# Kernel tuning notes

Measured on AMD Instinct MI355X. Metric: run time of the kernel, lower is better.

The kernel has to match this reference:

```python
import jax, jax.numpy as jnp
import numpy as np


def _dequant_linear(x, wq, scale):
    # wq: int [out, in], scale: [out] per-output-channel
    w = wq.astype(jnp.float32) * scale[:, None]  # dequantize
    return jnp.einsum('bsh,oh->bso', x, w)


def setup_inputs() -> dict:
    key = jax.random.key(0)
    ks = jax.random.split(key, 7)
    B, S, H, I = 2, 2048, 4096, 14336
    x = jax.random.normal(ks[0], (B, S, H), dtype=jnp.float32)
    gate_wq = jax.random.randint(ks[1], (I, H), -128, 128, dtype=jnp.int32)
    up_wq = jax.random.randint(ks[2], (I, H), -128, 128, dtype=jnp.int32)
    down_wq = jax.random.randint(ks[3], (H, I), -128, 128, dtype=jnp.int32)
    # small positive per-channel scales (~1/(127*sqrt(fan_in)))
    gate_scale = jax.random.uniform(ks[4], (I,), dtype=jnp.float32, minval=0.5, maxval=1.5) / (127.0 * np.sqrt(H))
    up_scale = jax.random.uniform(ks[5], (I,), dtype=jnp.float32, minval=0.5, maxval=1.5) / (127.0 * np.sqrt(H))
    down_scale = jax.random.uniform(ks[6], (H,), dtype=jnp.float32, minval=0.5, maxval=1.5) / (127.0 * np.sqrt(I))
    return {'x': x, 'gate_wq': gate_wq, 'gate_scale': gate_scale,
            'up_wq': up_wq, 'up_scale': up_scale,
            'down_wq': down_wq, 'down_scale': down_scale}


def reference(x, gate_wq, gate_scale, up_wq, up_scale, down_wq, down_scale):
    gate = _dequant_linear(x, gate_wq, gate_scale)   # [B,S,I]
    up = _dequant_linear(x, up_wq, up_scale)         # [B,S,I]
    h = jax.nn.silu(gate) * up                       # SwiGLU
    return _dequant_linear(h, down_wq, down_scale)   # [B,S,H]
```

## Files before the change

kernel.cpp:

```cpp
#include <hip/hip_runtime.h>

typedef __bf16 bf16x8 __attribute__((ext_vector_type(8)));
typedef float f32x4 __attribute__((ext_vector_type(4)));

__device__ __forceinline__ unsigned short f2bf(float f) {
  unsigned u = __float_as_uint(f);
  u += 0x7FFFu + ((u >> 16) & 1u);
  return (unsigned short)(u >> 16);
}

__device__ __forceinline__ void async16(const void* g, void* l) {
  __builtin_amdgcn_global_load_lds((const __attribute__((address_space(1))) void*)g,
                                   (__attribute__((address_space(3))) void*)l,
                                   16, 0, 0);
}

__global__ void cvt_f32_bf16_k(const float4* __restrict__ in, ushort4* __restrict__ out) {
  int i = blockIdx.x * blockDim.x + threadIdx.x;
  float4 v = in[i];
  ushort4 o;
  o.x = f2bf(v.x); o.y = f2bf(v.y); o.z = f2bf(v.z); o.w = f2bf(v.w);
  out[i] = o;
}

__global__ void cvt_i32_bf16_k(const int4* __restrict__ in, ushort4* __restrict__ out) {
  int i = blockIdx.x * blockDim.x + threadIdx.x;
  int4 v = in[i];
  ushort4 o;
  o.x = f2bf((float)v.x); o.y = f2bf((float)v.y);
  o.z = f2bf((float)v.z); o.w = f2bf((float)v.w);
  out[i] = o;
}

__global__ __launch_bounds__(256, 2)
void gemm_gateup(const unsigned short* __restrict__ A,
                 const unsigned short* __restrict__ Bg,
                 const unsigned short* __restrict__ Bu,
                 const float* __restrict__ gsc, const float* __restrict__ usc,
                 unsigned short* __restrict__ Hout,
                 int M, int N, int K) {
  __shared__ unsigned short sA[128 * 64];
  __shared__ unsigned short sBg[128 * 64];
  __shared__ unsigned short sBu[128 * 64];

  const int tid  = threadIdx.x;
  const int lane = tid & 63;
  const int wv   = tid >> 6;

  const int bid = blockIdx.x;
  const int grp = bid >> 8;
  const int rem = bid & 255;
  const int bN  = ((grp << 3) + (rem & 7)) * 128;
  const int bM  = (rem >> 3) * 128;

  const int srow = lane >> 3;
  const int gcol = ((lane & 7) ^ srow) * 8;

  const unsigned short* gA  = A  + (size_t)(bM + wv * 32 + srow) * K + gcol;
  const unsigned short* gBg = Bg + (size_t)(bN + wv * 32 + srow) * K + gcol;
  const unsigned short* gBu = Bu + (size_t)(bN + wv * 32 + srow) * K + gcol;
  unsigned short* lA  = &sA [(wv * 32) * 64];
  unsigned short* lBg = &sBg[(wv * 32) * 64];
  unsigned short* lBu = &sBu[(wv * 32) * 64];

  const int r  = lane & 15;
  const int q  = lane >> 4;
  const int rx = r & 7;
  const int wm = (wv >> 1) * 64;
  const int wn = (wv & 1) * 64;

  f32x4 accg[4][4], accu[4][4];
#pragma unroll
  for (int i = 0; i < 4; i++)
#pragma unroll
    for (int j = 0; j < 4; j++) {
      accg[i][j] = f32x4{0.f, 0.f, 0.f, 0.f};
      accu[i][j] = f32x4{0.f, 0.f, 0.f, 0.f};
    }

  for (int k0 = 0; k0 < K; k0 += 64) {
    const unsigned short* pA = gA + k0;
    async16(pA,                  lA);
    async16(pA +  8 * (size_t)K, lA +  8 * 64);
    async16(pA + 16 * (size_t)K, lA + 16 * 64);
    async16(pA + 24 * (size_t)K, lA + 24 * 64);
    const unsigned short* pG = gBg + k0;
    async16(pG,                  lBg);
    async16(pG +  8 * (size_t)K, lBg +  8 * 64);
    async16(pG + 16 * (size_t)K, lBg + 16 * 64);
    async16(pG + 24 * (size_t)K, lBg + 24 * 64);
    const unsigned short* pU = gBu + k0;
    async16(pU,                  lBu);
    async16(pU +  8 * (size_t)K, lBu +  8 * 64);
    async16(pU + 16 * (size_t)K, lBu + 16 * 64);
    async16(pU + 24 * (size_t)K, lBu + 24 * 64);
    __syncthreads();

#pragma unroll
    for (int kk = 0; kk < 2; ++kk) {
      const int pc = ((kk * 4 + q) ^ rx) * 8;
      bf16x8 af[4];
#pragma unroll
      for (int mi = 0; mi < 4; mi++)
        af[mi] = *(const bf16x8*)&sA[(wm + mi * 16 + r) * 64 + pc];
#pragma unroll
      for (int ni = 0; ni < 4; ni++) {
        bf16x8 bg = *(const bf16x8*)&sBg[(wn + ni * 16 + r) * 64 + pc];
        bf16x8 bu = *(const bf16x8*)&sBu[(wn + ni * 16 + r) * 64 + pc];
#pragma unroll
        for (int mi = 0; mi < 4; mi++) {
          accg[mi][ni] = __builtin_amdgcn_mfma_f32_16x16x32_bf16(af[mi], bg, accg[mi][ni], 0, 0, 0);
          accu[mi][ni] = __builtin_amdgcn_mfma_f32_16x16x32_bf16(af[mi], bu, accu[mi][ni], 0, 0, 0);
        }
      }
    }
    __syncthreads();
  }

#pragma unroll
  for (int ni = 0; ni < 4; ni++) {
    const int col = bN + wn + ni * 16 + r;
    const float gs = gsc[col], us = usc[col];
#pragma unroll
    for (int mi = 0; mi < 4; mi++) {
#pragma unroll
      for (int rr = 0; rr < 4; rr++) {
        const int row = bM + wm + mi * 16 + q * 4 + rr;
        float g = accg[mi][ni][rr] * gs;
        float u = accu[mi][ni][rr] * us;
        float hv = (g / (1.f + __expf(-g))) * u;
        Hout[(size_t)row * N + col] = f2bf(hv);
      }
    }
  }
}

#define BAR() do { asm volatile("" ::: "memory"); __builtin_amdgcn_s_barrier(); \
                   asm volatile("" ::: "memory"); } while (0)

#define STAGE2(GP, LP) do { async16((GP), (LP)); \
    async16((GP) + 8 * (size_t)K, (LP) + 8 * 64); } while (0)

#define LOAD_A(AF, CURA, HA)                                                   \
  _Pragma("unroll") for (int mi = 0; mi < 4; ++mi)                             \
  _Pragma("unroll") for (int kk = 0; kk < 2; ++kk)                             \
    AF[mi][kk] = *(const bf16x8*)&(CURA)[((HA) * 128 + wrow + mi * 16 + r) * 64 \
                                         + (((kk * 4 + q) ^ rx) * 8)];

#define LOAD_B(BF, CURB, HB)                                                   \
  _Pragma("unroll") for (int ni = 0; ni < 2; ++ni)                             \
  _Pragma("unroll") for (int kk = 0; kk < 2; ++kk)                             \
    BF[ni][kk] = *(const bf16x8*)&(CURB)[((HB) * 128 + wcol + ni * 16 + r) * 64 \
                                         + (((kk * 4 + q) ^ rx) * 8)];

#define MFMA16(ACC, AF, BF)                                                    \
  __builtin_amdgcn_s_setprio(1);                                               \
  _Pragma("unroll") for (int kk = 0; kk < 2; ++kk)                             \
  _Pragma("unroll") for (int ni = 0; ni < 2; ++ni)                             \
  _Pragma("unroll") for (int mi = 0; mi < 4; ++mi)                             \
    ACC[mi][ni] = __builtin_amdgcn_mfma_f32_16x16x32_bf16(                     \
        AF[mi][kk], BF[ni][kk], ACC[mi][ni], 0, 0, 0);                         \
  __builtin_amdgcn_s_setprio(0);

__global__ __launch_bounds__(512, 2)
void gemm_down(const unsigned short* __restrict__ A,
               const unsigned short* __restrict__ B,
               const float* __restrict__ dsc,
               float* __restrict__ out,
               int M, int N, int K) {
  __shared__ unsigned short sA[2 * 256 * 64];
  __shared__ unsigned short sB[2 * 256 * 64];

  const int tid  = threadIdx.x;
  const int lane = tid & 63;
  const int wv   = tid >> 6;

  const int bid  = blockIdx.x;
  const int wgid = (bid & 7) * 32 + (bid >> 3);
  const int bM = (wgid >> 4) * 256;
  const int bN = (wgid & 15) * 256;

  const int srow = lane >> 3;
  const int gcol = ((lane & 7) ^ srow) * 8;

  const unsigned short* gA0 = A + (size_t)(bM +       wv * 16 + srow) * K + gcol;
  const unsigned short* gA1 = A + (size_t)(bM + 128 + wv * 16 + srow) * K + gcol;
  const unsigned short* gB0 = B + (size_t)(bN +       wv * 16 + srow) * K + gcol;
  const unsigned short* gB1 = B + (size_t)(bN + 128 + wv * 16 + srow) * K + gcol;

  const int r    = lane & 15;
  const int q    = lane >> 4;
  const int rx   = r & 7;
  const int wrow = (wv >> 2) * 64;
  const int wcol = (wv & 3) * 32;

  f32x4 a00[4][2], a01[4][2], a10[4][2], a11[4][2];
#pragma unroll
  for (int i = 0; i < 4; i++)
#pragma unroll
    for (int j = 0; j < 2; j++) {
      a00[i][j] = f32x4{0.f, 0.f, 0.f, 0.f};
      a01[i][j] = f32x4{0.f, 0.f, 0.f, 0.f};
      a10[i][j] = f32x4{0.f, 0.f, 0.f, 0.f};
      a11[i][j] = f32x4{0.f, 0.f, 0.f, 0.f};
    }

  const int NT = K >> 6;

  STAGE2(gA0, &sA[ wv * 16 * 64]);
  STAGE2(gB0, &sB[ wv * 16 * 64]);
  STAGE2(gB1, &sB[(128 + wv * 16) * 64]);
  STAGE2(gA1, &sA[(128 + wv * 16) * 64]);
  asm volatile("s_waitcnt vmcnt(4)" ::: "memory");
  __builtin_amdgcn_s_barrier();

  int cur = 0;
  for (int t = 0; t < NT; ++t) {
    const unsigned short* curA = sA + cur * (256 * 64);
    const unsigned short* curB = sB + cur * (256 * 64);
    unsigned short* nxtA = sA + (cur ^ 1) * (256 * 64);
    unsigned short* nxtB = sB + (cur ^ 1) * (256 * 64);
    const int  kn = (t + 1) << 6;
    const bool st = (t + 1) < NT;

    bf16x8 af0[4][2], af1[4][2];

    {
      bf16x8 bfr[2][2];
      LOAD_A(af0, curA, 0);
      LOAD_B(bfr, curB, 0);
      if (st) STAGE2(gA0 + kn, nxtA + wv * 16 * 64);
      BAR();
      MFMA16(a00, af0, bfr);
      if (st) asm volatile("s_waitcnt vmcnt(4)" ::: "memory");
      else    asm volatile("s_waitcnt vmcnt(2)" ::: "memory");
      BAR();
    }
    {
      bf16x8 bfr[2][2];
      LOAD_B(bfr, curB, 1);
      if (st) STAGE2(gB0 + kn, nxtB + wv * 16 * 64);
      BAR();
      MFMA16(a01, af0, bfr);
      if (st) asm volatile("s_waitcnt vmcnt(4)" ::: "memory");
      else    asm volatile("s_waitcnt vmcnt(0)" ::: "memory");
      BAR();
    }
    {
      bf16x8 bfr[2][2];
      LOAD_A(af1, curA, 1);
      LOAD_B(bfr, curB, 0);
      if (st) STAGE2(gB1 + kn, nxtB + (128 + wv * 16) * 64);
      BAR();
      MFMA16(a10, af1, bfr);
      BAR();
    }
    {
      bf16x8 bfr[2][2];
      LOAD_B(bfr, curB, 1);
      if (st) STAGE2(gA1 + kn, nxtA + (128 + wv * 16) * 64);
      BAR();
      MFMA16(a11, af1, bfr);
      if (st) {
        asm volatile("s_waitcnt vmcnt(4)" ::: "memory");
        BAR();
      }
    }
    cur ^= 1;
  }

#pragma unroll
  for (int ni = 0; ni < 2; ++ni) {
    const int c0 = bN + wcol + ni * 16 + r;
    const int c1 = c0 + 128;
    const float s0 = dsc[c0], s1 = dsc[c1];
#pragma unroll
    for (int mi = 0; mi < 4; ++mi) {
#pragma unroll
      for (int rr = 0; rr < 4; ++rr) {
        const int row0 = bM + wrow + mi * 16 + q * 4 + rr;
        const int row1 = row0 + 128;
        out[(size_t)row0 * N + c0] = a00[mi][ni][rr] * s0;
        out[(size_t)row0 * N + c1] = a01[mi][ni][rr] * s1;
        out[(size_t)row1 * N + c0] = a10[mi][ni][rr] * s0;
        out[(size_t)row1 * N + c1] = a11[mi][ni][rr] * s1;
      }
    }
  }
}

extern "C" void kernel_launch(void* const* d_in, const int* in_sizes, int n_in,
                              void* d_out, int out_size, void* d_ws, size_t ws_size,
                              hipStream_t stream) {
  constexpr int M  = 4096;
  constexpr int Hd = 4096;
  constexpr int Id = 14336;

  const float* x   = (const float*)d_in[0];
  const int*   gwq = (const int*)  d_in[1];
  const float* gsc = (const float*)d_in[2];
  const int*   uwq = (const int*)  d_in[3];
  const float* usc = (const float*)d_in[4];
  const int*   dwq = (const int*)  d_in[5];
  const float* dsc = (const float*)d_in[6];
  float* out = (float*)d_out;

  unsigned short* xb = (unsigned short*)d_ws;
  unsigned short* w0 = xb + (size_t)M * Hd;
  unsigned short* wu = w0 + (size_t)Id * Hd;
  unsigned short* hb = wu + (size_t)Id * Hd;

  cvt_f32_bf16_k<<<(M * Hd) / 1024, 256, 0, stream>>>((const float4*)x, (ushort4*)xb);
  cvt_i32_bf16_k<<<((size_t)Id * Hd) / 1024, 256, 0, stream>>>((const int4*)gwq, (ushort4*)w0);
  cvt_i32_bf16_k<<<((size_t)Id * Hd) / 1024, 256, 0, stream>>>((const int4*)uwq, (ushort4*)wu);

  gemm_gateup<<<(Id / 128) * (M / 128), 256, 0, stream>>>(xb, w0, wu, gsc, usc, hb, M, Id, Hd);

  cvt_i32_bf16_k<<<((size_t)Hd * Id) / 1024, 256, 0, stream>>>((const int4*)dwq, (ushort4*)w0);

  gemm_down<<<(M / 256) * (Hd / 256), 512, 0, stream>>>(hb, w0, dsc, out, M, Hd, Id);
}
```

Measured before the change: 2.063 ms.

## Deepen down-proj GEMM prefetch to two tiles ahead with in-place buffer refill

The down-projection GEMM main loop is restructured so that global-to-LDS loads for tile t+2 are issued into the current buffer as soon as each quarter is consumed, with three-and-a-half tiles primed before the loop. Wait counts are raised (vmcnt 8/10) and an explicit lgkmcnt(0) is added before each MFMA group, and the quadrant order is changed to reuse B fragments. The intent is to hide more global memory latency behind MFMA work. It adds a separate drain loop for the last two tiles and relies on intricate barrier/waitcnt correctness when overwriting buffers that are still being read.

```diff
diff --git a/kernel.cpp b/kernel.cpp
--- a/kernel.cpp
+++ b/kernel.cpp
@@ -137,6 +137,10 @@
 
 #define BAR() do { asm volatile("" ::: "memory"); __builtin_amdgcn_s_barrier(); \
                    asm volatile("" ::: "memory"); } while (0)
+#define LGKM0 asm volatile("s_waitcnt lgkmcnt(0)" ::: "memory")
+#define VM8   asm volatile("s_waitcnt vmcnt(8)"  ::: "memory")
+#define VM10  asm volatile("s_waitcnt vmcnt(10)" ::: "memory")
+#define VM0   asm volatile("s_waitcnt vmcnt(0)"  ::: "memory")
 
 #define STAGE2(GP, LP) do { async16((GP), (LP)); \
     async16((GP) + 8 * (size_t)K, (LP) + 8 * 64); } while (0)
@@ -168,8 +172,9 @@
                const float* __restrict__ dsc,
                float* __restrict__ out,
                int M, int N, int K) {
-  __shared__ unsigned short sA[2 * 256 * 64];
-  __shared__ unsigned short sB[2 * 256 * 64];
+  constexpr int TS = 256 * 64;
+  __shared__ unsigned short sA[2 * TS];
+  __shared__ unsigned short sB[2 * TS];
 
   const int tid  = threadIdx.x;
   const int lane = tid & 63;
@@ -207,66 +212,75 @@
 
   const int NT = K >> 6;
 
-  STAGE2(gA0, &sA[ wv * 16 * 64]);
-  STAGE2(gB0, &sB[ wv * 16 * 64]);
-  STAGE2(gB1, &sB[(128 + wv * 16) * 64]);
-  STAGE2(gA1, &sA[(128 + wv * 16) * 64]);
-  asm volatile("s_waitcnt vmcnt(4)" ::: "memory");
+  STAGE2(gA0,      &sA[       (wv * 16) * 64]);
+  STAGE2(gB0,      &sB[       (wv * 16) * 64]);
+  STAGE2(gA1,      &sA[(128 + wv * 16) * 64]);
+  STAGE2(gB1,      &sB[(128 + wv * 16) * 64]);
+  STAGE2(gA0 + 64, &sA[TS +        (wv * 16) * 64]);
+  STAGE2(gB0 + 64, &sB[TS +        (wv * 16) * 64]);
+  STAGE2(gA1 + 64, &sA[TS + (128 + wv * 16) * 64]);
+  VM10;
   __builtin_amdgcn_s_barrier();
 
-  int cur = 0;
-  for (int t = 0; t < NT; ++t) {
-    const unsigned short* curA = sA + cur * (256 * 64);
-    const unsigned short* curB = sB + cur * (256 * 64);
-    unsigned short* nxtA = sA + (cur ^ 1) * (256 * 64);
-    unsigned short* nxtB = sB + (cur ^ 1) * (256 * 64);
-    const int  kn = (t + 1) << 6;
-    const bool st = (t + 1) < NT;
-
-    bf16x8 af0[4][2], af1[4][2];
-
-    {
-      bf16x8 bfr[2][2];
-      LOAD_A(af0, curA, 0);
-      LOAD_B(bfr, curB, 0);
-      if (st) STAGE2(gA0 + kn, nxtA + wv * 16 * 64);
-      BAR();
-      MFMA16(a00, af0, bfr);
-      if (st) asm volatile("s_waitcnt vmcnt(4)" ::: "memory");
-      else    asm volatile("s_waitcnt vmcnt(2)" ::: "memory");
-      BAR();
-    }
-    {
-      bf16x8 bfr[2][2];
-      LOAD_B(bfr, curB, 1);
-      if (st) STAGE2(gB0 + kn, nxtB + wv * 16 * 64);
-      BAR();
-      MFMA16(a01, af0, bfr);
-      if (st) asm volatile("s_waitcnt vmcnt(4)" ::: "memory");
-      else    asm volatile("s_waitcnt vmcnt(0)" ::: "memory");
-      BAR();
-    }
-    {
-      bf16x8 bfr[2][2];
-      LOAD_A(af1, curA, 1);
-      LOAD_B(bfr, curB, 0);
-      if (st) STAGE2(gB1 + kn, nxtB + (128 + wv * 16) * 64);
-      BAR();
-      MFMA16(a10, af1, bfr);
-      BAR();
-    }
-    {
-      bf16x8 bfr[2][2];
-      LOAD_B(bfr, curB, 1);
-      if (st) STAGE2(gA1 + kn, nxtA + (128 + wv * 16) * 64);
-      BAR();
-      MFMA16(a11, af1, bfr);
-      if (st) {
-        asm volatile("s_waitcnt vmcnt(4)" ::: "memory");
-        BAR();
-      }
-    }
-    cur ^= 1;
+  for (int t = 0; t < NT - 2; ++t) {
+    const int cb = t & 1;
+    const unsigned short* curA = sA + cb * TS;
+    const unsigned short* curB = sB + cb * TS;
+    unsigned short* cA = sA + cb * TS;
+    unsigned short* cB = sB + cb * TS;
+    unsigned short* nB = sB + (cb ^ 1) * TS;
+    const size_t k1 = (size_t)(t + 1) << 6;
+    const size_t k2 = (size_t)(t + 2) << 6;
+
+    bf16x8 af0[4][2], af1[4][2], b0[2][2], b1[2][2];
+
+    LOAD_A(af0, curA, 0);
+    LOAD_B(b0, curB, 0);
+    STAGE2(gB1 + k1, nB + (128 + wv * 16) * 64);
+    BAR(); LGKM0;
+    MFMA16(a00, af0, b0);
+    VM8; BAR();
+    LOAD_A(af1, curA, 1);
+    STAGE2(gA0 + k2, cA + (wv * 16) * 64);
+    BAR(); LGKM0;
+    MFMA16(a10, af1, b0);
+    VM8; BAR();
+    LOAD_B(b1, curB, 1);
+    STAGE2(gB0 + k2, cB + (wv * 16) * 64);
+    BAR(); LGKM0;
+    MFMA16(a01, af0, b1);
+    VM8; BAR();
+    STAGE2(gA1 + k2, cA + (128 + wv * 16) * 64);
+    BAR(); LGKM0;
+    MFMA16(a11, af1, b1);
+    VM8; BAR();
+  }
+
+  for (int t = NT - 2; t < NT; ++t) {
+    const int cb = t & 1;
+    const unsigned short* curA = sA + cb * TS;
+    const unsigned short* curB = sB + cb * TS;
+    unsigned short* nB = sB + (cb ^ 1) * TS;
+    const size_t k1 = (size_t)(t + 1) << 6;
+
+    bf16x8 af0[4][2], af1[4][2], b0[2][2], b1[2][2];
+
+    LOAD_A(af0, curA, 0);
+    LOAD_B(b0, curB, 0);
+    if (t + 1 < NT) STAGE2(gB1 + k1, nB + (128 + wv * 16) * 64);
+    VM0; BAR(); LGKM0;
+    MFMA16(a00, af0, b0);
+    BAR();
+    LOAD_A(af1, curA, 1);
+    BAR(); LGKM0;
+    MFMA16(a10, af1, b0);
+    BAR();
+    LOAD_B(b1, curB, 1);
+    BAR(); LGKM0;
+    MFMA16(a01, af0, b1);
+    BAR();
+    MFMA16(a11, af1, b1);
+    BAR();
   }
 
 #pragma unroll
```

New measurement: 2.055 ms. Within noise of the previous version (-0.4%).
